# Kernel optimization log

Measured on AMD Instinct MI355X. Metric: run time of the kernel, lower is better.

Reference implementation:

```python
import jax, jax.numpy as jnp
import numpy as np

DIM_EMB = 512
NB_HEADS = 16
NB_LAYERS = 3
BSZ = 256
NB_NODES = 500
NEG_INF = -1e9


def my_mha(q, K, V, nb_heads, mask=None, clip_value=None):
    # q: (bsz, 1, d); K, V: (bsz, n, d); mask: (bsz, n) bool (True = masked)
    bsz, n, d = K.shape
    dh = d // nb_heads
    qh = q.reshape(bsz, nb_heads, dh)            # split emb into heads
    Kh = K.reshape(bsz, n, nb_heads, dh)
    Vh = V.reshape(bsz, n, nb_heads, dh)
    scores = jnp.einsum('bhd,bnhd->bhn', qh, Kh) / jnp.sqrt(jnp.asarray(dh, q.dtype))
    if clip_value is not None:
        scores = clip_value * jnp.tanh(scores)
    if mask is not None:
        scores = jnp.where(mask[:, None, :], jnp.asarray(NEG_INF, scores.dtype), scores)
    w = jax.nn.softmax(scores, axis=-1)          # (bsz, H, n)
    out = jnp.einsum('bhn,bnhd->bhd', w, Vh).reshape(bsz, 1, d)
    attn_weights = w.mean(axis=1)[:, None, :]    # (bsz, 1, n)
    return out, attn_weights


def setup_inputs() -> dict:
    key = jax.random.key(0)
    ks = jax.random.split(key, 5)
    s = 1.0 / np.sqrt(DIM_EMB)
    return {
        'query': jax.random.normal(ks[0], (BSZ, 1, DIM_EMB), jnp.float32),
        'K_att': jax.random.normal(ks[1], (BSZ, NB_NODES, DIM_EMB * NB_LAYERS), jnp.float32),
        'V_att': jax.random.normal(ks[2], (BSZ, NB_NODES, DIM_EMB * NB_LAYERS), jnp.float32),
        'mask': jnp.zeros((BSZ, NB_NODES), jnp.bool_),
        'W0_w': jax.random.normal(ks[3], (DIM_EMB, DIM_EMB), jnp.float32) * s,
        'W0_b': jnp.zeros((DIM_EMB,), jnp.float32),
        'Wqf_w': jax.random.normal(ks[4], (DIM_EMB, DIM_EMB), jnp.float32) * s,
        'Wqf_b': jnp.zeros((DIM_EMB,), jnp.float32),
    }


def reference(query, K_att, V_att, mask, W0_w, W0_b, Wqf_w, Wqf_b):
    d = DIM_EMB
    attn_weights = None
    for l in range(NB_LAYERS):
        K_l = K_att[:, :, l * d:(l + 1) * d]
        V_l = V_att[:, :, l * d:(l + 1) * d]
        if l < NB_LAYERS - 1:
            out, _ = my_mha(query, K_l, V_l, NB_HEADS, mask)
            query = out @ W0_w.T + W0_b
        else:
            q_final = (query @ Wqf_w.T + Wqf_b).reshape(-1, 1, d)
            _, attn_weights = my_mha(q_final, K_l, V_l, 1, mask, clip_value=10.0)
    return attn_weights[:, 0, :]  # (bsz, nb_nodes)
```

## Files before the change

### kernel.cpp

```cpp
#include <hip/hip_runtime.h>
#include <cstdint>
#include <cstddef>

#define BSZ 256
#define NN 500
#define D 512
#define H 16
#define KSTRIDE 1536
#define NEG_INF -1000000000.0f

__global__ __launch_bounds__(256) void transpose512(
    const float* __restrict__ W0, const float* __restrict__ Wf,
    float* __restrict__ Wt0, float* __restrict__ Wtf)
{
    __shared__ float tile[32][33];
    const float* in = blockIdx.z ? Wf : W0;
    float* out      = blockIdx.z ? Wtf : Wt0;
    const int bx = blockIdx.x * 32, by = blockIdx.y * 32;
    const int tx = threadIdx.x, ty = threadIdx.y;
#pragma unroll
    for (int i = 0; i < 32; i += 8)
        tile[ty + i][tx] = in[(size_t)(by + ty + i) * D + bx + tx];
    __syncthreads();
#pragma unroll
    for (int i = 0; i < 32; i += 8)
        out[(size_t)(bx + ty + i) * D + by + tx] = tile[tx][ty + i];
}

__global__ __launch_bounds__(1024) void attn_layer_fused(
    const float* __restrict__ q_in,
    const float* __restrict__ Katt,
    const float* __restrict__ Vatt,
    const unsigned char* __restrict__ mask,
    const float* __restrict__ Wt,
    const float* __restrict__ bias,
    float* __restrict__ q_out,
    int loff)
{
    __shared__ __align__(16) float part_acc[16 * D];
    __shared__ float part_m[16 * H];
    __shared__ float part_l[16 * H];
    __shared__ __align__(16) float out_lds[D];
    __shared__ float gemv_part[2 * D];

    const int b = blockIdx.x;
    const int t = threadIdx.x;
    const int r = t & 63;
    const int g = t >> 6;

    const float* qp = q_in + (size_t)b * D + r * 8;
    const float4 qa = *reinterpret_cast<const float4*>(qp);
    const float4 qb = *reinterpret_cast<const float4*>(qp + 4);

    const float* Kb = Katt + (size_t)b * NN * KSTRIDE + loff;
    const float* Vb = Vatt + (size_t)b * NN * KSTRIDE + loff;
    const unsigned char* mb = mask + (size_t)b * NN;

    float m = -3.4e38f, lsum = 0.f;
    float4 acc0 = {0.f, 0.f, 0.f, 0.f};
    float4 acc1 = {0.f, 0.f, 0.f, 0.f};

#pragma unroll 2
    for (int n = g; n < NN; n += 16) {
        const float* kr = Kb + (size_t)n * KSTRIDE + r * 8;
        const float* vr = Vb + (size_t)n * KSTRIDE + r * 8;
        const float4 ka  = *reinterpret_cast<const float4*>(kr);
        const float4 kb4 = *reinterpret_cast<const float4*>(kr + 4);
        const float4 va  = *reinterpret_cast<const float4*>(vr);
        const float4 vb4 = *reinterpret_cast<const float4*>(vr + 4);

        float s = qa.x * ka.x + qa.y * ka.y + qa.z * ka.z + qa.w * ka.w
                + qb.x * kb4.x + qb.y * kb4.y + qb.z * kb4.z + qb.w * kb4.w;
        s += __shfl_xor(s, 1);
        s += __shfl_xor(s, 2);
        float sc = s * 0.17677669529663687f;
        if (mb[n]) sc = NEG_INF;

        const float mn   = fmaxf(m, sc);
        const float corr = __expf(m - mn);
        const float e    = __expf(sc - mn);
        lsum = lsum * corr + e;
        acc0.x = acc0.x * corr + e * va.x;
        acc0.y = acc0.y * corr + e * va.y;
        acc0.z = acc0.z * corr + e * va.z;
        acc0.w = acc0.w * corr + e * va.w;
        acc1.x = acc1.x * corr + e * vb4.x;
        acc1.y = acc1.y * corr + e * vb4.y;
        acc1.z = acc1.z * corr + e * vb4.z;
        acc1.w = acc1.w * corr + e * vb4.w;
        m = mn;
    }

    *reinterpret_cast<float4*>(part_acc + g * D + r * 8)     = acc0;
    *reinterpret_cast<float4*>(part_acc + g * D + r * 8 + 4) = acc1;
    if ((r & 3) == 0) {
        part_m[g * H + (r >> 2)] = m;
        part_l[g * H + (r >> 2)] = lsum;
    }
    __syncthreads();

    if (t < D) {
        const int hd = t >> 5;
        float ms = -3.4e38f;
#pragma unroll
        for (int g2 = 0; g2 < 16; ++g2)
            ms = fmaxf(ms, part_m[g2 * H + hd]);
        float ls = 0.f, o = 0.f;
#pragma unroll
        for (int g2 = 0; g2 < 16; ++g2) {
            const float w = __expf(part_m[g2 * H + hd] - ms);
            ls += part_l[g2 * H + hd] * w;
            o  += part_acc[g2 * D + t] * w;
        }
        out_lds[t] = o / ls;
    }
    __syncthreads();

    {
        const int j = t & 511;
        const int half = t >> 9;
        const float* Wp = Wt + (size_t)half * 256 * D + j;
        const float* a  = out_lds + half * 256;
        float acc = 0.f;
#pragma unroll 4
        for (int k = 0; k < 256; ++k)
            acc += a[k] * Wp[(size_t)k * D];
        gemv_part[half * D + j] = acc;
    }
    __syncthreads();
    if (t < D)
        q_out[(size_t)b * D + t] = gemv_part[t] + gemv_part[D + t] + bias[t];
}

__global__ __launch_bounds__(1024) void final_layer(
    const float* __restrict__ q_in,
    const float* __restrict__ Katt,
    const unsigned char* __restrict__ mask,
    const float* __restrict__ Wt,
    const float* __restrict__ bias,
    float* __restrict__ out)
{
    __shared__ float a_lds[D];
    __shared__ __align__(16) float qf_lds[D];
    __shared__ float part2[2 * D];
    __shared__ float s_lds[NN];
    __shared__ float red[16];
    __shared__ float bm, bs;

    const int b = blockIdx.x;
    const int t = threadIdx.x;

    if (t < D) a_lds[t] = q_in[(size_t)b * D + t];
    __syncthreads();

    {
        const int j = t & 511;
        const int half = t >> 9;
        const float* Wp = Wt + (size_t)half * 256 * D + j;
        const float* a  = a_lds + half * 256;
        float acc = 0.f;
#pragma unroll 4
        for (int k = 0; k < 256; ++k)
            acc += a[k] * Wp[(size_t)k * D];
        part2[half * D + j] = acc;
    }
    __syncthreads();
    if (t < D) qf_lds[t] = part2[t] + part2[D + t] + bias[t];
    __syncthreads();

    const int wv   = t >> 6;
    const int l    = t & 63;
    const int half = l >> 5;
    const int l32  = l & 31;

    const float* qpp = qf_lds + l32 * 16;
    const float4 q0 = *reinterpret_cast<const float4*>(qpp);
    const float4 q1 = *reinterpret_cast<const float4*>(qpp + 4);
    const float4 q2 = *reinterpret_cast<const float4*>(qpp + 8);
    const float4 q3 = *reinterpret_cast<const float4*>(qpp + 12);

    const float* Kb = Katt + (size_t)b * NN * KSTRIDE + 1024;
    const unsigned char* mb = mask + (size_t)b * NN;

    for (int n = wv * 2 + half; n < NN; n += 32) {
        const float* kr = Kb + (size_t)n * KSTRIDE + l32 * 16;
        const float4 k0 = *reinterpret_cast<const float4*>(kr);
        const float4 k1 = *reinterpret_cast<const float4*>(kr + 4);
        const float4 k2 = *reinterpret_cast<const float4*>(kr + 8);
        const float4 k3 = *reinterpret_cast<const float4*>(kr + 12);
        float s = q0.x * k0.x + q0.y * k0.y + q0.z * k0.z + q0.w * k0.w
                + q1.x * k1.x + q1.y * k1.y + q1.z * k1.z + q1.w * k1.w
                + q2.x * k2.x + q2.y * k2.y + q2.z * k2.z + q2.w * k2.w
                + q3.x * k3.x + q3.y * k3.y + q3.z * k3.z + q3.w * k3.w;
#pragma unroll
        for (int o = 1; o < 32; o <<= 1) s += __shfl_xor(s, o);
        if (l32 == 0) {
            float sc = 10.0f * tanhf(s * 0.044194173824159216f);
            if (mb[n]) sc = NEG_INF;
            s_lds[n] = sc;
        }
    }
    __syncthreads();

    const float v = (t < NN) ? s_lds[t] : -3.4e38f;
    float m = v;
#pragma unroll
    for (int o = 1; o < 64; o <<= 1) m = fmaxf(m, __shfl_xor(m, o));
    if (l == 0) red[wv] = m;
    __syncthreads();
    if (t == 0) {
        float mm = red[0];
#pragma unroll
        for (int i = 1; i < 16; ++i) mm = fmaxf(mm, red[i]);
        bm = mm;
    }
    __syncthreads();
    const float e = (t < NN) ? __expf(v - bm) : 0.f;
    float ssum = e;
#pragma unroll
    for (int o = 1; o < 64; o <<= 1) ssum += __shfl_xor(ssum, o);
    if (l == 0) red[wv] = ssum;
    __syncthreads();
    if (t == 0) {
        float s2 = 0.f;
#pragma unroll
        for (int i = 0; i < 16; ++i) s2 += red[i];
        bs = 1.0f / s2;
    }
    __syncthreads();
    if (t < NN) out[(size_t)b * NN + t] = e * bs;
}

extern "C" void kernel_launch(void* const* d_in, const int* in_sizes, int n_in,
                              void* d_out, int out_size, void* d_ws, size_t ws_size,
                              hipStream_t stream) {
    const float* query = (const float*)d_in[0];
    const float* Katt  = (const float*)d_in[1];
    const float* Vatt  = (const float*)d_in[2];
    const unsigned char* mask = (const unsigned char*)d_in[3];
    const float* W0w = (const float*)d_in[4];
    const float* W0b = (const float*)d_in[5];
    const float* Wfw = (const float*)d_in[6];
    const float* Wfb = (const float*)d_in[7];

    float* out = (float*)d_out;
    float* ws  = (float*)d_ws;
    float* q1  = ws;
    float* q2  = ws + 131072;
    float* Wt0 = ws + 262144;
    float* Wtf = ws + 524288;

    transpose512<<<dim3(16, 16, 2), dim3(32, 8), 0, stream>>>(W0w, Wfw, Wt0, Wtf);
    attn_layer_fused<<<BSZ, 1024, 0, stream>>>(query, Katt, Vatt, mask, Wt0, W0b, q1, 0);
    attn_layer_fused<<<BSZ, 1024, 0, stream>>>(q1,    Katt, Vatt, mask, Wt0, W0b, q2, 512);
    final_layer<<<BSZ, 1024, 0, stream>>>(q2, Katt, mask, Wtf, Wfb, out);
}
```

Baseline: 309.4 us.

## Split attention over node halves across two blocks and merge with separate kernels

Each batch's attention is split across two 512-thread blocks, each covering half of the nodes. They write partial accumulators and softmax stats to workspace, and separate combine/GEMV and merge kernels finish the work. The final query projection is folded into the second layer's combine kernel, so the final attention kernel only does scores and softmax. This doubles the block count to improve CU occupancy on a 256-block grid. In exchange it adds more kernel launches and extra global round-trips for the partial results.

After: 349.0 us. 12.8% more time.

```diff
diff --git a/kernel.cpp b/kernel.cpp
--- a/kernel.cpp
+++ b/kernel.cpp
@@ -4,10 +4,21 @@
 
 #define BSZ 256
 #define NN 500
+#define NH 250
 #define D 512
 #define H 16
 #define KSTRIDE 1536
 #define NEG_INF -1000000000.0f
+
+#define WS_Q1    0
+#define WS_QF    131072
+#define WS_WT0   262144
+#define WS_WTF   524288
+#define WS_PACC  786432
+#define WS_PM    1048576
+#define WS_PL    1056768
+#define WS_E     786432
+#define WS_SM    1048576
 
 __global__ __launch_bounds__(256) void transpose512(
     const float* __restrict__ W0, const float* __restrict__ Wf,
@@ -27,23 +38,22 @@
         out[(size_t)(bx + ty + i) * D + by + tx] = tile[tx][ty + i];
 }
 
-__global__ __launch_bounds__(1024) void attn_layer_fused(
+__global__ __launch_bounds__(512) void attn_partial(
     const float* __restrict__ q_in,
     const float* __restrict__ Katt,
     const float* __restrict__ Vatt,
     const unsigned char* __restrict__ mask,
-    const float* __restrict__ Wt,
-    const float* __restrict__ bias,
-    float* __restrict__ q_out,
+    float* __restrict__ pacc,
+    float* __restrict__ pm,
+    float* __restrict__ pl,
     int loff)
 {
-    __shared__ __align__(16) float part_acc[16 * D];
-    __shared__ float part_m[16 * H];
-    __shared__ float part_l[16 * H];
-    __shared__ __align__(16) float out_lds[D];
-    __shared__ float gemv_part[2 * D];
-
-    const int b = blockIdx.x;
+    __shared__ __align__(16) float part_acc[8 * D];
+    __shared__ float part_m[8 * H];
+    __shared__ float part_l[8 * H];
+
+    const int hhalf = blockIdx.x;
+    const int b = blockIdx.y;
     const int t = threadIdx.x;
     const int r = t & 63;
     const int g = t >> 6;
@@ -56,12 +66,15 @@
     const float* Vb = Vatt + (size_t)b * NN * KSTRIDE + loff;
     const unsigned char* mb = mask + (size_t)b * NN;
 
+    const int n0 = hhalf * NH;
+    const int n1 = n0 + NH;
+
     float m = -3.4e38f, lsum = 0.f;
     float4 acc0 = {0.f, 0.f, 0.f, 0.f};
     float4 acc1 = {0.f, 0.f, 0.f, 0.f};
 
 #pragma unroll 2
-    for (int n = g; n < NN; n += 16) {
+    for (int n = n0 + g; n < n1; n += 8) {
         const float* kr = Kb + (size_t)n * KSTRIDE + r * 8;
         const float* vr = Vb + (size_t)n * KSTRIDE + r * 8;
         const float4 ka  = *reinterpret_cast<const float4*>(kr);
@@ -99,27 +112,59 @@
     }
     __syncthreads();
 
-    if (t < D) {
+    {
         const int hd = t >> 5;
         float ms = -3.4e38f;
 #pragma unroll
-        for (int g2 = 0; g2 < 16; ++g2)
+        for (int g2 = 0; g2 < 8; ++g2)
             ms = fmaxf(ms, part_m[g2 * H + hd]);
         float ls = 0.f, o = 0.f;
 #pragma unroll
-        for (int g2 = 0; g2 < 16; ++g2) {
+        for (int g2 = 0; g2 < 8; ++g2) {
             const float w = __expf(part_m[g2 * H + hd] - ms);
             ls += part_l[g2 * H + hd] * w;
             o  += part_acc[g2 * D + t] * w;
         }
-        out_lds[t] = o / ls;
+        const size_t pb = (size_t)(b * 2 + hhalf);
+        pacc[pb * D + t] = o;
+        if ((t & 31) == 0) {
+            pm[pb * H + hd] = ms;
+            pl[pb * H + hd] = ls;
+        }
+    }
+}
+
+__global__ __launch_bounds__(1024) void combine_gemv(
+    const float* __restrict__ pacc,
+    const float* __restrict__ pm,
+    const float* __restrict__ pl,
+    const float* __restrict__ Wt1, const float* __restrict__ b1,
+    const float* __restrict__ Wt2, const float* __restrict__ b2,
+    float* __restrict__ q_out, int dbl)
+{
+    __shared__ __align__(16) float out_lds[D];
+    __shared__ __align__(16) float mid_lds[D];
+    __shared__ float gemv_part[2 * D];
+
+    const int b = blockIdx.x;
+    const int t = threadIdx.x;
+
+    if (t < D) {
+        const int hd = t >> 5;
+        const size_t p0 = (size_t)(b * 2 + 0);
+        const size_t p1 = (size_t)(b * 2 + 1);
+        const float m0 = pm[p0 * H + hd], m1 = pm[p1 * H + hd];
+        const float M  = fmaxf(m0, m1);
+        const float w0 = __expf(m0 - M), w1 = __expf(m1 - M);
+        const float l  = pl[p0 * H + hd] * w0 + pl[p1 * H + hd] * w1;
+        out_lds[t] = (pacc[p0 * D + t] * w0 + pacc[p1 * D + t] * w1) / l;
     }
     __syncthreads();
 
     {
         const int j = t & 511;
         const int half = t >> 9;
-        const float* Wp = Wt + (size_t)half * 256 * D + j;
+        const float* Wp = Wt1 + (size_t)half * 256 * D + j;
         const float* a  = out_lds + half * 256;
         float acc = 0.f;
 #pragma unroll 4
@@ -128,81 +173,78 @@
         gemv_part[half * D + j] = acc;
     }
     __syncthreads();
-    if (t < D)
-        q_out[(size_t)b * D + t] = gemv_part[t] + gemv_part[D + t] + bias[t];
-}
-
-__global__ __launch_bounds__(1024) void final_layer(
-    const float* __restrict__ q_in,
-    const float* __restrict__ Katt,
-    const unsigned char* __restrict__ mask,
-    const float* __restrict__ Wt,
-    const float* __restrict__ bias,
-    float* __restrict__ out)
-{
-    __shared__ float a_lds[D];
-    __shared__ __align__(16) float qf_lds[D];
-    __shared__ float part2[2 * D];
-    __shared__ float s_lds[NN];
-    __shared__ float red[16];
-    __shared__ float bm, bs;
-
-    const int b = blockIdx.x;
-    const int t = threadIdx.x;
-
-    if (t < D) a_lds[t] = q_in[(size_t)b * D + t];
+    if (t < D) mid_lds[t] = gemv_part[t] + gemv_part[D + t] + b1[t];
+
+    if (!dbl) {
+        if (t < D) q_out[(size_t)b * D + t] = mid_lds[t];
+        return;
+    }
     __syncthreads();
 
     {
         const int j = t & 511;
         const int half = t >> 9;
-        const float* Wp = Wt + (size_t)half * 256 * D + j;
-        const float* a  = a_lds + half * 256;
+        const float* Wp = Wt2 + (size_t)half * 256 * D + j;
+        const float* a  = mid_lds + half * 256;
         float acc = 0.f;
 #pragma unroll 4
         for (int k = 0; k < 256; ++k)
             acc += a[k] * Wp[(size_t)k * D];
-        part2[half * D + j] = acc;
-    }
-    __syncthreads();
-    if (t < D) qf_lds[t] = part2[t] + part2[D + t] + bias[t];
-    __syncthreads();
-
-    const int wv   = t >> 6;
-    const int l    = t & 63;
-    const int half = l >> 5;
-    const int l32  = l & 31;
-
-    const float* qpp = qf_lds + l32 * 16;
-    const float4 q0 = *reinterpret_cast<const float4*>(qpp);
-    const float4 q1 = *reinterpret_cast<const float4*>(qpp + 4);
-    const float4 q2 = *reinterpret_cast<const float4*>(qpp + 8);
-    const float4 q3 = *reinterpret_cast<const float4*>(qpp + 12);
+        gemv_part[half * D + j] = acc;
+    }
+    __syncthreads();
+    if (t < D)
+        q_out[(size_t)b * D + t] = gemv_part[t] + gemv_part[D + t] + b2[t];
+}
+
+__global__ __launch_bounds__(512) void final_partial(
+    const float* __restrict__ qf,
+    const float* __restrict__ Katt,
+    const unsigned char* __restrict__ mask,
+    float* __restrict__ e_ws,
+    float* __restrict__ sm_ws)
+{
+    __shared__ __align__(16) float q_lds[D];
+    __shared__ float s_lds[NH];
+    __shared__ float red[8];
+    __shared__ float bm;
+
+    const int hhalf = blockIdx.x;
+    const int b = blockIdx.y;
+    const int t = threadIdx.x;
+    const int l = t & 63;
+    const int wv = t >> 6;
+
+    q_lds[t] = qf[(size_t)b * D + t];
+    __syncthreads();
+
+    const float* qp = q_lds + l * 8;
+    const float4 q0 = *reinterpret_cast<const float4*>(qp);
+    const float4 q1 = *reinterpret_cast<const float4*>(qp + 4);
 
     const float* Kb = Katt + (size_t)b * NN * KSTRIDE + 1024;
     const unsigned char* mb = mask + (size_t)b * NN;
-
-    for (int n = wv * 2 + half; n < NN; n += 32) {
-        const float* kr = Kb + (size_t)n * KSTRIDE + l32 * 16;
+    const int n0 = hhalf * NH;
+
+#pragma unroll 2
+    for (int nl = wv; nl < NH; nl += 8) {
+        const int n = n0 + nl;
+        const float* kr = Kb + (size_t)n * KSTRIDE + l * 8;
         const float4 k0 = *reinterpret_cast<const float4*>(kr);
         const float4 k1 = *reinterpret_cast<const float4*>(kr + 4);
-        const float4 k2 = *reinterpret_cast<const float4*>(kr + 8);
-        const float4 k3 = *reinterpret_cast<const float4*>(kr + 12);
         float s = q0.x * k0.x + q0.y * k0.y + q0.z * k0.z + q0.w * k0.w
-                + q1.x * k1.x + q1.y * k1.y + q1.z * k1.z + q1.w * k1.w
-                + q2.x * k2.x + q2.y * k2.y + q2.z * k2.z + q2.w * k2.w
-                + q3.x * k3.x + q3.y * k3.y + q3.z * k3.z + q3.w * k3.w;
-#pragma unroll
-        for (int o = 1; o < 32; o <<= 1) s += __shfl_xor(s, o);
-        if (l32 == 0) {
+                + q1.x * k1.x + q1.y * k1.y + q1.z * k1.z + q1.w * k1.w;
+#pragma unroll
+        for (int o = 1; o < 64; o <<= 1) s += __shfl_xor(s, o);
+        if (l == 0) {
             float sc = 10.0f * tanhf(s * 0.044194173824159216f);
             if (mb[n]) sc = NEG_INF;
-            s_lds[n] = sc;
+            s_lds[nl] = sc;
         }
     }
     __syncthreads();
 
-    const float v = (t < NN) ? s_lds[t] : -3.4e38f;
+    const float v = (t < NH) ? s_lds[t] : -3.4e38f;
     float m = v;
 #pragma unroll
     for (int o = 1; o < 64; o <<= 1) m = fmaxf(m, __shfl_xor(m, o));
@@ -211,24 +253,50 @@
     if (t == 0) {
         float mm = red[0];
 #pragma unroll
-        for (int i = 1; i < 16; ++i) mm = fmaxf(mm, red[i]);
+        for (int i = 1; i < 8; ++i) mm = fmaxf(mm, red[i]);
         bm = mm;
     }
     __syncthreads();
-    const float e = (t < NN) ? __expf(v - bm) : 0.f;
+    const float e = (t < NH) ? __expf(v - bm) : 0.f;
     float ssum = e;
 #pragma unroll
     for (int o = 1; o < 64; o <<= 1) ssum += __shfl_xor(ssum, o);
     if (l == 0) red[wv] = ssum;
     __syncthreads();
+
+    const size_t pb = (size_t)(b * 2 + hhalf);
+    if (t < NH) e_ws[pb * 256 + t] = e;
     if (t == 0) {
         float s2 = 0.f;
 #pragma unroll
-        for (int i = 0; i < 16; ++i) s2 += red[i];
-        bs = 1.0f / s2;
-    }
-    __syncthreads();
-    if (t < NN) out[(size_t)b * NN + t] = e * bs;
+        for (int i = 0; i < 8; ++i) s2 += red[i];
+        sm_ws[pb * 2]     = bm;
+        sm_ws[pb * 2 + 1] = s2;
+    }
+}
+
+__global__ __launch_bounds__(512) void final_merge(
+    const float* __restrict__ e_ws,
+    const float* __restrict__ sm_ws,
+    float* __restrict__ out)
+{
+    const int b = blockIdx.x;
+    const int t = threadIdx.x;
+
+    const float m0 = sm_ws[(size_t)(b * 2) * 2];
+    const float s0 = sm_ws[(size_t)(b * 2) * 2 + 1];
+    const float m1 = sm_ws[(size_t)(b * 2 + 1) * 2];
+    const float s1 = sm_ws[(size_t)(b * 2 + 1) * 2 + 1];
+    const float M  = fmaxf(m0, m1);
+    const float w0 = __expf(m0 - M), w1 = __expf(m1 - M);
+    const float inv = 1.0f / (s0 * w0 + s1 * w1);
+
+    if (t < NN) {
+        const int h = (t >= NH) ? 1 : 0;
+        const int idx = t - h * NH;
+        const float e = e_ws[(size_t)(b * 2 + h) * 256 + idx];
+        out[(size_t)b * NN + t] = e * (h ? w1 : w0) * inv;
+    }
 }
 
 extern "C" void kernel_launch(void* const* d_in, const int* in_sizes, int n_in,
@@ -245,13 +313,28 @@
 
     float* out = (float*)d_out;
     float* ws  = (float*)d_ws;
-    float* q1  = ws;
-    float* q2  = ws + 131072;
-    float* Wt0 = ws + 262144;
-    float* Wtf = ws + 524288;
+    float* q1   = ws + WS_Q1;
+    float* qf   = ws + WS_QF;
+    float* Wt0  = ws + WS_WT0;
+    float* Wtf  = ws + WS_WTF;
+    float* pacc = ws + WS_PACC;
+    float* pm   = ws + WS_PM;
+    float* pl   = ws + WS_PL;
+    float* e_ws = ws + WS_E;
+    float* sm   = ws + WS_SM;
 
     transpose512<<<dim3(16, 16, 2), dim3(32, 8), 0, stream>>>(W0w, Wfw, Wt0, Wtf);
-    attn_layer_fused<<<BSZ, 1024, 0, stream>>>(query, Katt, Vatt, mask, Wt0, W0b, q1, 0);
-    attn_layer_fused<<<BSZ, 1024, 0, stream>>>(q1,    Katt, Vatt, mask, Wt0, W0b, q2, 512);
-    final_layer<<<BSZ, 1024, 0, stream>>>(q2, Katt, mask, Wtf, Wfb, out);
-}
+
+    attn_partial<<<dim3(2, BSZ), 512, 0, stream>>>(query, Katt, Vatt, mask,
+                                                   pacc, pm, pl, 0);
+    combine_gemv<<<BSZ, 1024, 0, stream>>>(pacc, pm, pl, Wt0, W0b,
+                                           nullptr, nullptr, q1, 0);
+
+    attn_partial<<<dim3(2, BSZ), 512, 0, stream>>>(q1, Katt, Vatt, mask,
+                                                   pacc, pm, pl, 512);
+    combine_gemv<<<BSZ, 1024, 0, stream>>>(pacc, pm, pl, Wt0, W0b,
+                                           Wtf, Wfb, qf, 1);
+
+    final_partial<<<dim3(2, BSZ), 512, 0, stream>>>(qf, Katt, mask, e_ws, sm);
+    final_merge<<<BSZ, 512, 0, stream>>>(e_ws, sm, out);
+}
```
